# Optimization experiments

Hardware: AMD Instinct MI355X
Metric: run time of the kernel (lower is better)

Reference implementation:

```python
import jax, jax.numpy as jnp
import numpy as np

OBS_DIM, ACT_DIM, HIDDEN, BATCH = 1024, 8, 64, 131072
BLOCK = 16  # NVFP4 quantization block size along the input dim
FP4_GRID = jnp.array([0.0, 0.5, 1.0, 1.5, 2.0, 3.0, 4.0, 6.0], dtype=jnp.float32)


def nvfp4_dequant(w):
    """Simulated NVFP4: per-16-elem-block absmax/6 scale, round to E2M1 grid, dequant."""
    out_f, in_f = w.shape
    wb = w.reshape(out_f, in_f // BLOCK, BLOCK)
    scale = jnp.max(jnp.abs(wb), axis=-1, keepdims=True) / 6.0
    scale = jnp.where(scale == 0, 1.0, scale)
    x = wb / scale
    idx = jnp.argmin(jnp.abs(jnp.abs(x)[..., None] - FP4_GRID), axis=-1)
    q = jnp.sign(x) * FP4_GRID[idx]
    return (q * scale).reshape(out_f, in_f)


def setup_inputs() -> dict:
    key = jax.random.key(0)
    ks = jax.random.split(key, 6)
    obs = jax.random.normal(ks[0], (BATCH, OBS_DIM), dtype=jnp.float32)
    # orthogonal-ish init approximated with scaled normals (values irrelevant to correctness harness)
    w_in = jax.random.normal(ks[1], (HIDDEN, OBS_DIM), dtype=jnp.float32) * (np.sqrt(2.0) / np.sqrt(OBS_DIM))
    b_in = jnp.zeros((HIDDEN,), dtype=jnp.float32)
    w_h1 = jax.random.normal(ks[2], (HIDDEN, HIDDEN), dtype=jnp.float32) / np.sqrt(HIDDEN)
    b_h1 = jnp.zeros((HIDDEN,), dtype=jnp.float32)
    w_pi = jax.random.normal(ks[3], (ACT_DIM, HIDDEN), dtype=jnp.float32) * (0.01 / np.sqrt(HIDDEN))
    b_pi = jnp.zeros((ACT_DIM,), dtype=jnp.float32)
    w_v = jax.random.normal(ks[4], (1, HIDDEN), dtype=jnp.float32) / np.sqrt(HIDDEN)
    b_v = jnp.zeros((1,), dtype=jnp.float32)
    log_std = jnp.full((ACT_DIM,), -0.5, dtype=jnp.float32)
    return {"obs": obs, "w_in": w_in, "b_in": b_in, "w_h1": w_h1, "b_h1": b_h1,
            "w_pi": w_pi, "b_pi": b_pi, "w_v": w_v, "b_v": b_v, "log_std": log_std}


def reference(obs, w_in, b_in, w_h1, b_h1, w_pi, b_pi, w_v, b_v, log_std):
    x = jnp.tanh(obs @ w_in.T + b_in)                 # [B, H]
    w_h1_dq = nvfp4_dequant(w_h1)                     # fp4 fake-quant weight
    z = jnp.tanh(x @ w_h1_dq.T + b_h1)                # [B, H]
    mean = z @ w_pi.T + b_pi                          # [B, A]
    value = (z @ w_v.T + b_v)[:, 0]                   # [B]
    std = jnp.broadcast_to(jnp.exp(log_std), mean.shape)
    return mean, std, value
```

## Files before the change

kernel.cpp:

```cpp
#include <hip/hip_runtime.h>
#include <hip/hip_bf16.h>

#define OBS_DIM 1024
#define ACT_DIM 8
#define HIDDEN  64
#define BATCH   131072
#define NBLOCKS (BATCH / 64)
#define KCHUNK  128
#define NCHUNK  (OBS_DIM / KCHUNK)

typedef short bf16x8 __attribute__((ext_vector_type(8)));
typedef short bf16x4 __attribute__((ext_vector_type(4)));
typedef float f32x4  __attribute__((ext_vector_type(4)));

__device__ __forceinline__ ushort f2bf(float f) {
    union { __hip_bfloat16 h; ushort u; } c;
    c.h = __float2bfloat16(f);
    return c.u;
}

__device__ __forceinline__ float fast_tanh(float x) {
    float e = __expf(2.0f * x);
    return 1.0f - 2.0f / (e + 1.0f);
}

__device__ __forceinline__ bf16x8 pack8(float4 a, float4 b) {
    bf16x8 r;
    r[0] = (short)f2bf(a.x); r[1] = (short)f2bf(a.y);
    r[2] = (short)f2bf(a.z); r[3] = (short)f2bf(a.w);
    r[4] = (short)f2bf(b.x); r[5] = (short)f2bf(b.y);
    r[6] = (short)f2bf(b.z); r[7] = (short)f2bf(b.w);
    return r;
}

__global__ __launch_bounds__(256) void w_in_to_bf16(const float* __restrict__ w_in,
                                                    ushort* __restrict__ wbf) {
    const int i = (blockIdx.x * 256 + threadIdx.x) * 4;
    float4 v = *(const float4*)&w_in[i];
    ushort4 o;
    o.x = f2bf(v.x); o.y = f2bf(v.y); o.z = f2bf(v.z); o.w = f2bf(v.w);
    *(ushort4*)&wbf[i] = o;
}

template <bool USE_WS>
__global__ __launch_bounds__(256) void ac_mfma(
    const float* __restrict__ obs,  const float* __restrict__ w_in,
    const float* __restrict__ b_in, const float* __restrict__ w_h1,
    const float* __restrict__ b_h1, const float* __restrict__ w_pi,
    const float* __restrict__ b_pi, const float* __restrict__ w_v,
    const float* __restrict__ b_v,  const float* __restrict__ log_std,
    const ushort* __restrict__ wbf, float* __restrict__ out)
{
    __shared__ __align__(16) ushort smem[16384];

    const int tid = threadIdx.x;
    const int w   = tid >> 6;
    const int l   = tid & 63;
    const int lr  = l & 15;
    const int lg  = l >> 4;
    const int row0 = blockIdx.x * 64;

    const int srow = tid >> 5;
    const int scol = (tid & 31) * 4;
    const int sswz = srow << 3;

    const size_t bbase = (size_t)(w * 16 + lr) * OBS_DIM + lg * 8;

    float4 sv[8];
    bf16x8 regB[2][4];

#define LOADC(kc)                                                                  \
    _Pragma("unroll")                                                              \
    for (int i = 0; i < 8; ++i) {                                                  \
        const int row = i * 8 + srow;                                              \
        sv[i] = *(const float4*)&obs[(size_t)(row0 + row) * OBS_DIM +              \
                                     (kc) * KCHUNK + scol];                        \
    }

#define BLOAD(kc)                                                                  \
    _Pragma("unroll")                                                              \
    for (int s = 0; s < 4; ++s) {                                                  \
        if constexpr (USE_WS) {                                                    \
            regB[(kc) & 1][s] = *(const bf16x8*)(wbf + bbase +                     \
                                                 ((kc) * 4 + s) * 32);             \
        } else {                                                                   \
            const float* bp = w_in + bbase + ((kc) * 4 + s) * 32;                  \
            regB[(kc) & 1][s] = pack8(*(const float4*)bp, *(const float4*)(bp+4)); \
        }                                                                          \
    }

#define STOREC(kc)                                                                 \
    _Pragma("unroll")                                                              \
    for (int i = 0; i < 8; ++i) {                                                  \
        const int row = i * 8 + srow;                                              \
        bf16x4 v4;                                                                 \
        v4[0] = (short)f2bf(sv[i].x); v4[1] = (short)f2bf(sv[i].y);                \
        v4[2] = (short)f2bf(sv[i].z); v4[3] = (short)f2bf(sv[i].w);                \
        *(bf16x4*)&smem[((kc) & 1) * 8192 + row * 128 + (scol ^ sswz)] = v4;       \
    }

#define COMPUTE(kc)                                                                \
    {                                                                              \
        const int bb = ((kc) & 1) * 8192;                                          \
        _Pragma("unroll")                                                          \
        for (int s = 0; s < 4; ++s) {                                              \
            _Pragma("unroll")                                                      \
            for (int rt = 0; rt < 4; ++rt) {                                       \
                const int arow = rt * 16 + lr;                                     \
                bf16x8 af = *(const bf16x8*)&smem[bb + arow * 128 +                \
                                ((s * 32 + lg * 8) ^ ((arow & 7) << 3))];          \
                acc[rt] = __builtin_amdgcn_mfma_f32_16x16x32_bf16(                 \
                              af, regB[(kc) & 1][s], acc[rt], 0, 0, 0);            \
            }                                                                      \
        }                                                                          \
    }

    f32x4 acc[4];
    #pragma unroll
    for (int t = 0; t < 4; ++t) acc[t] = (f32x4){0.f, 0.f, 0.f, 0.f};

    LOADC(0)
    BLOAD(0)
    STOREC(0)
    __syncthreads();
    #pragma unroll
    for (int kc = 1; kc < NCHUNK; ++kc) {
        LOADC(kc)
        COMPUTE(kc - 1)
        BLOAD(kc)
        STOREC(kc)
        __syncthreads();
    }
    COMPUTE(NCHUNK - 1)
    __syncthreads();

    ushort* x_lds = smem;
    ushort* z_lds = smem + 4608;
    ushort* wdq   = smem + 9216;
    ushort* wh    = smem + 13824;

    {
        const float b = b_in[w * 16 + lr];
        #pragma unroll
        for (int rt = 0; rt < 4; ++rt)
            #pragma unroll
            for (int r = 0; r < 4; ++r)
                x_lds[(rt * 16 + lg * 4 + r) * 72 + w * 16 + lr] =
                    f2bf(fast_tanh(acc[rt][r] + b));
    }

    {
        const int o  = tid >> 2;
        const int hb = tid & 3;
        const float* wp = w_h1 + o * HIDDEN + hb * 16;
        float v[16];
        #pragma unroll
        for (int i = 0; i < 4; ++i) {
            float4 t4 = *(const float4*)(wp + i * 4);
            v[i*4+0] = t4.x; v[i*4+1] = t4.y; v[i*4+2] = t4.z; v[i*4+3] = t4.w;
        }
        float amax = 0.f;
        #pragma unroll
        for (int i = 0; i < 16; ++i) amax = fmaxf(amax, fabsf(v[i]));
        float scale = amax / 6.0f;
        if (scale == 0.f) scale = 1.f;
        #pragma unroll
        for (int i = 0; i < 16; ++i) {
            float xq = v[i] / scale;
            float ax = fabsf(xq);
            float q;
            if      (ax <= 0.25f) q = 0.0f;
            else if (ax <= 0.75f) q = 0.5f;
            else if (ax <= 1.25f) q = 1.0f;
            else if (ax <= 1.75f) q = 1.5f;
            else if (ax <= 2.5f)  q = 2.0f;
            else if (ax <= 3.5f)  q = 3.0f;
            else if (ax <= 5.0f)  q = 4.0f;
            else                  q = 6.0f;
            q = (xq < 0.f) ? -q : q;
            wdq[o * 72 + hb * 16 + i] = f2bf(q * scale);
        }
    }
    for (int t2 = tid; t2 < 16 * 64; t2 += 256) {
        const int o = t2 >> 6, h = t2 & 63;
        float val = (o < 8) ? w_pi[o * HIDDEN + h] : (o == 8 ? w_v[h] : 0.0f);
        wh[o * 72 + h] = f2bf(val);
    }
    __syncthreads();

    f32x4 acc2[4];
    #pragma unroll
    for (int t = 0; t < 4; ++t) acc2[t] = (f32x4){0.f, 0.f, 0.f, 0.f};
    #pragma unroll
    for (int ks = 0; ks < 2; ++ks) {
        bf16x8 af = *(const bf16x8*)&x_lds[(w * 16 + lr) * 72 + ks * 32 + lg * 8];
        #pragma unroll
        for (int t = 0; t < 4; ++t) {
            bf16x8 bfr = *(const bf16x8*)&wdq[(t * 16 + lr) * 72 + ks * 32 + lg * 8];
            acc2[t] = __builtin_amdgcn_mfma_f32_16x16x32_bf16(af, bfr, acc2[t], 0, 0, 0);
        }
    }
    #pragma unroll
    for (int t = 0; t < 4; ++t) {
        const float b = b_h1[t * 16 + lr];
        #pragma unroll
        for (int r = 0; r < 4; ++r)
            z_lds[(w * 16 + lg * 4 + r) * 72 + t * 16 + lr] = f2bf(fast_tanh(acc2[t][r] + b));
    }
    __syncthreads();

    f32x4 acc3 = (f32x4){0.f, 0.f, 0.f, 0.f};
    #pragma unroll
    for (int ks = 0; ks < 2; ++ks) {
        bf16x8 af  = *(const bf16x8*)&z_lds[(w * 16 + lr) * 72 + ks * 32 + lg * 8];
        bf16x8 bfr = *(const bf16x8*)&wh[lr * 72 + ks * 32 + lg * 8];
        acc3 = __builtin_amdgcn_mfma_f32_16x16x32_bf16(af, bfr, acc3, 0, 0, 0);
    }
    #pragma unroll
    for (int r = 0; r < 4; ++r) {
        const int row = row0 + w * 16 + lg * 4 + r;
        if (lr < 8)
            out[(size_t)row * 8 + lr] = acc3[r] + b_pi[lr];
        else if (lr == 8)
            out[(size_t)2 * BATCH * 8 + row] = acc3[r] + b_v[0];
    }

    {
        const int idx = tid * 2;
        const int rl = idx >> 3, a = idx & 7;
        float2 s;
        s.x = __expf(log_std[a]);
        s.y = __expf(log_std[a + 1]);
        *(float2*)&out[(size_t)BATCH * 8 + (size_t)(row0 + rl) * 8 + a] = s;
    }
#undef LOADC
#undef BLOAD
#undef STOREC
#undef COMPUTE
}

extern "C" void kernel_launch(void* const* d_in, const int* in_sizes, int n_in,
                              void* d_out, int out_size, void* d_ws, size_t ws_size,
                              hipStream_t stream) {
    (void)in_sizes; (void)n_in; (void)out_size;
    const float* obs   = (const float*)d_in[0];
    const float* w_in  = (const float*)d_in[1];
    const float* b_in  = (const float*)d_in[2];
    const float* w_h1  = (const float*)d_in[3];
    const float* b_h1  = (const float*)d_in[4];
    const float* w_pi  = (const float*)d_in[5];
    const float* b_pi  = (const float*)d_in[6];
    const float* w_v   = (const float*)d_in[7];
    const float* b_v   = (const float*)d_in[8];
    const float* lstd  = (const float*)d_in[9];
    float* out = (float*)d_out;

    const size_t wbf_bytes = (size_t)HIDDEN * OBS_DIM * sizeof(ushort);
    if (ws_size >= wbf_bytes) {
        ushort* wbf = (ushort*)d_ws;
        hipLaunchKernelGGL(w_in_to_bf16, dim3(HIDDEN * OBS_DIM / 1024), dim3(256), 0, stream,
                           w_in, wbf);
        hipLaunchKernelGGL((ac_mfma<true>), dim3(NBLOCKS), dim3(256), 0, stream,
                           obs, w_in, b_in, w_h1, b_h1, w_pi, b_pi, w_v, b_v, lstd,
                           wbf, out);
    } else {
        hipLaunchKernelGGL((ac_mfma<false>), dim3(NBLOCKS), dim3(256), 0, stream,
                           obs, w_in, b_in, w_h1, b_h1, w_pi, b_pi, w_v, b_v, lstd,
                           (const ushort*)nullptr, out);
    }
}
```

Before: 121.2 us.

## Deepen obs prefetch to two chunks with double register staging

The first-layer K loop now keeps two register staging buffers, so global loads for chunk kc+1 are issued a full iteration ahead of their LDS store, and the loop is manually unrolled by two. Scheduling barriers keep the weight and obs loads grouped ahead of the MFMA compute. The aim is to hide HBM latency on the obs stream, which dominates this memory-bound kernel. The cost is doubled staging registers (64 more VGPRs), which may reduce occupancy.

```diff
diff --git a/kernel.cpp b/kernel.cpp
--- a/kernel.cpp
+++ b/kernel.cpp
@@ -66,10 +66,10 @@
 
     const size_t bbase = (size_t)(w * 16 + lr) * OBS_DIM + lg * 8;
 
-    float4 sv[8];
+    float4 svA[8], svB[8];
     bf16x8 regB[2][4];
 
-#define LOADC(kc)                                                                  \
+#define LOADC(kc, sv)                                                              \
     _Pragma("unroll")                                                              \
     for (int i = 0; i < 8; ++i) {                                                  \
         const int row = i * 8 + srow;                                              \
@@ -89,7 +89,7 @@
         }                                                                          \
     }
 
-#define STOREC(kc)                                                                 \
+#define STOREC(kc, sv)                                                             \
     _Pragma("unroll")                                                              \
     for (int i = 0; i < 8; ++i) {                                                  \
         const int row = i * 8 + srow;                                              \
@@ -115,22 +115,35 @@
         }                                                                          \
     }
 
+#define VMEM_FENCE() __builtin_amdgcn_sched_barrier(0x106)
+
     f32x4 acc[4];
     #pragma unroll
     for (int t = 0; t < 4; ++t) acc[t] = (f32x4){0.f, 0.f, 0.f, 0.f};
 
-    LOADC(0)
     BLOAD(0)
-    STOREC(0)
-    __syncthreads();
-    #pragma unroll
-    for (int kc = 1; kc < NCHUNK; ++kc) {
-        LOADC(kc)
+    LOADC(0, svA)
+    LOADC(1, svB)
+    STOREC(0, svA)
+    __syncthreads();
+    for (int kc = 1; kc < NCHUNK - 1; kc += 2) {
+        BLOAD(kc)
+        VMEM_FENCE();
+        LOADC(kc + 1, svA)
         COMPUTE(kc - 1)
-        BLOAD(kc)
-        STOREC(kc)
+        STOREC(kc, svB)
         __syncthreads();
-    }
+        BLOAD(kc + 1)
+        VMEM_FENCE();
+        LOADC(kc + 2, svB)
+        COMPUTE(kc)
+        STOREC(kc + 1, svA)
+        __syncthreads();
+    }
+    BLOAD(NCHUNK - 1)
+    COMPUTE(NCHUNK - 2)
+    STOREC(NCHUNK - 1, svB)
+    __syncthreads();
     COMPUTE(NCHUNK - 1)
     __syncthreads();
 
@@ -237,6 +250,7 @@
 #undef BLOAD
 #undef STOREC
 #undef COMPUTE
+#undef VMEM_FENCE
 }
 
 extern "C" void kernel_launch(void* const* d_in, const int* in_sizes, int n_in,
```

New measurement: 112.7 us. -7.0%, faster.

## Double K-chunk to 256 and remap obs loads to wave-per-row coalesced layout

Applied to the files above, without the earlier changes.

Raises the K chunk for the first layer from 128 to 256, halving the number of pipeline stages and __syncthreads barriers, and doubles the LDS staging buffer to 64 KB. Observation loads are remapped so each wave reads whole contiguous 1 KB row segments, and the B fragments are no longer double-buffered in registers. The larger LDS footprint and 16 float4 staging registers per thread may reduce occupancy. Dropping the regB double buffer could also expose weight-load latency before the MFMAs.

```diff
diff --git a/kernel.cpp b/kernel.cpp
--- a/kernel.cpp
+++ b/kernel.cpp
@@ -6,7 +6,7 @@
 #define HIDDEN  64
 #define BATCH   131072
 #define NBLOCKS (BATCH / 64)
-#define KCHUNK  128
+#define KCHUNK  256
 #define NCHUNK  (OBS_DIM / KCHUNK)
 
 typedef short bf16x8 __attribute__((ext_vector_type(8)));
@@ -51,7 +51,7 @@
     const float* __restrict__ b_v,  const float* __restrict__ log_std,
     const ushort* __restrict__ wbf, float* __restrict__ out)
 {
-    __shared__ __align__(16) ushort smem[16384];
+    __shared__ __align__(16) ushort smem[32768];
 
     const int tid = threadIdx.x;
     const int w   = tid >> 6;
@@ -60,57 +60,52 @@
     const int lg  = l >> 4;
     const int row0 = blockIdx.x * 64;
 
-    const int srow = tid >> 5;
-    const int scol = (tid & 31) * 4;
-    const int sswz = srow << 3;
-
     const size_t bbase = (size_t)(w * 16 + lr) * OBS_DIM + lg * 8;
-
-    float4 sv[8];
-    bf16x8 regB[2][4];
+    const float* aptr = obs + (size_t)(row0 + w) * OBS_DIM + l * 4;
+
+    float4 sv[16];
+    bf16x8 regB[8];
 
 #define LOADC(kc)                                                                  \
     _Pragma("unroll")                                                              \
-    for (int i = 0; i < 8; ++i) {                                                  \
-        const int row = i * 8 + srow;                                              \
-        sv[i] = *(const float4*)&obs[(size_t)(row0 + row) * OBS_DIM +              \
-                                     (kc) * KCHUNK + scol];                        \
+    for (int i = 0; i < 16; ++i) {                                                 \
+        sv[i] = *(const float4*)(aptr + (size_t)i * 4 * OBS_DIM + (kc) * KCHUNK);  \
     }
 
 #define BLOAD(kc)                                                                  \
     _Pragma("unroll")                                                              \
-    for (int s = 0; s < 4; ++s) {                                                  \
+    for (int s = 0; s < 8; ++s) {                                                  \
         if constexpr (USE_WS) {                                                    \
-            regB[(kc) & 1][s] = *(const bf16x8*)(wbf + bbase +                     \
-                                                 ((kc) * 4 + s) * 32);             \
+            regB[s] = *(const bf16x8*)(wbf + bbase + (kc) * KCHUNK + s * 32);      \
         } else {                                                                   \
-            const float* bp = w_in + bbase + ((kc) * 4 + s) * 32;                  \
-            regB[(kc) & 1][s] = pack8(*(const float4*)bp, *(const float4*)(bp+4)); \
+            const float* bp = w_in + bbase + (kc) * KCHUNK + s * 32;               \
+            regB[s] = pack8(*(const float4*)bp, *(const float4*)(bp + 4));         \
         }                                                                          \
     }
 
 #define STOREC(kc)                                                                 \
     _Pragma("unroll")                                                              \
-    for (int i = 0; i < 8; ++i) {                                                  \
-        const int row = i * 8 + srow;                                              \
+    for (int i = 0; i < 16; ++i) {                                                 \
+        const int row = i * 4 + w;                                                 \
         bf16x4 v4;                                                                 \
         v4[0] = (short)f2bf(sv[i].x); v4[1] = (short)f2bf(sv[i].y);                \
         v4[2] = (short)f2bf(sv[i].z); v4[3] = (short)f2bf(sv[i].w);                \
-        *(bf16x4*)&smem[((kc) & 1) * 8192 + row * 128 + (scol ^ sswz)] = v4;       \
+        *(bf16x4*)&smem[((kc) & 1) * 16384 + row * 256 +                           \
+                        ((l * 4) ^ ((row & 7) << 3))] = v4;                        \
     }
 
 #define COMPUTE(kc)                                                                \
     {                                                                              \
-        const int bb = ((kc) & 1) * 8192;                                          \
+        const int bb = ((kc) & 1) * 16384;                                         \
+        const int kswz = (lr & 7) << 3;                                            \
         _Pragma("unroll")                                                          \
-        for (int s = 0; s < 4; ++s) {                                              \
+        for (int s = 0; s < 8; ++s) {                                              \
             _Pragma("unroll")                                                      \
             for (int rt = 0; rt < 4; ++rt) {                                       \
-                const int arow = rt * 16 + lr;                                     \
-                bf16x8 af = *(const bf16x8*)&smem[bb + arow * 128 +                \
-                                ((s * 32 + lg * 8) ^ ((arow & 7) << 3))];          \
+                bf16x8 af = *(const bf16x8*)&smem[bb + (rt * 16 + lr) * 256 +      \
+                                ((s * 32 + lg * 8) ^ kswz)];                       \
                 acc[rt] = __builtin_amdgcn_mfma_f32_16x16x32_bf16(                 \
-                              af, regB[(kc) & 1][s], acc[rt], 0, 0, 0);            \
+                              af, regB[s], acc[rt], 0, 0, 0);                      \
             }                                                                      \
         }                                                                          \
     }
@@ -124,11 +119,11 @@
     STOREC(0)
     __syncthreads();
     #pragma unroll
-    for (int kc = 1; kc < NCHUNK; ++kc) {
-        LOADC(kc)
-        COMPUTE(kc - 1)
-        BLOAD(kc)
-        STOREC(kc)
+    for (int kc = 0; kc < NCHUNK - 1; ++kc) {
+        LOADC(kc + 1)
+        COMPUTE(kc)
+        BLOAD(kc + 1)
+        STOREC(kc + 1)
         __syncthreads();
     }
     COMPUTE(NCHUNK - 1)
```

New measurement: 132.3 us. 1.09x slower.
